# Kernel tuning notes

Measured on AMD Instinct MI355X. Metric: run time of the kernel, lower is better.

## Reference

```python
import jax, jax.numpy as jnp
import numpy as np
from jax import lax

BATCH = 8192
HIDDEN = 128
N_POINTS = 8
MAX_STEPS = 8     # adaptive substep budget per output interval
RTOL, ATOL = 1e-3, 1e-4

# Dormand-Prince 5(4) tableau (FSAL)
A21 = 1/5
A31, A32 = 3/40, 9/40
A41, A42, A43 = 44/45, -56/15, 32/9
A51, A52, A53, A54 = 19372/6561, -25360/2187, 64448/6561, -212/729
A61, A62, A63, A64, A65 = 9017/3168, -355/33, 46732/5247, 49/176, -5103/18656
B1, B3, B4, B5, B6 = 35/384, 500/1113, 125/192, -2187/6784, 11/84
# error weights = b(5th) - b(4th)
E1 = 35/384 - 5179/57600
E3 = 500/1113 - 7571/16695
E4 = 125/192 - 393/640
E5 = -2187/6784 + 92097/339200
E6 = 11/84 - 187/2100
E7 = -1/40


def setup_inputs() -> dict:
    key = jax.random.key(0)
    ks = jax.random.split(key, 6)
    def xavier(k, fi, fo):
        return (jax.random.normal(k, (fi, fo)) * jnp.sqrt(2.0 / (fi + fo))).astype(jnp.float32)
    W1 = xavier(ks[0], 2, HIDDEN); b1 = jnp.zeros((HIDDEN,), jnp.float32)
    W2 = xavier(ks[1], HIDDEN, HIDDEN); b2 = jnp.zeros((HIDDEN,), jnp.float32)
    W3 = xavier(ks[2], HIDDEN, HIDDEN); b3 = jnp.zeros((HIDDEN,), jnp.float32)
    W4 = xavier(ks[3], HIDDEN, 2); b4 = jnp.zeros((2,), jnp.float32)
    x0 = jax.random.normal(ks[4], (BATCH, 2), jnp.float32)
    t = (jnp.arange(N_POINTS, dtype=jnp.float32) * 0.1)
    return {"x0": x0, "t": t, "W1": W1, "b1": b1, "W2": W2, "b2": b2,
            "W3": W3, "b3": b3, "W4": W4, "b4": b4}


def _odeint(x0, t, W1, b1, W2, b2, W3, b3, W4, b4):
    def f(y):  # autonomous dynamics: ODEFunc ignores t
        h = jax.nn.elu(y @ W1 + b1)
        h = jax.nn.elu(h @ W2 + b2)
        h = jax.nn.elu(h @ W3 + b3)
        return h @ W4 + b4

    def dopri5_step(y, h):
        k1 = f(y)
        k2 = f(y + h * (A21 * k1))
        k3 = f(y + h * (A31 * k1 + A32 * k2))
        k4 = f(y + h * (A41 * k1 + A42 * k2 + A43 * k3))
        k5 = f(y + h * (A51 * k1 + A52 * k2 + A53 * k3 + A54 * k4))
        k6 = f(y + h * (A61 * k1 + A62 * k2 + A63 * k3 + A64 * k4 + A65 * k5))
        y5 = y + h * (B1 * k1 + B3 * k3 + B4 * k4 + B5 * k5 + B6 * k6)
        k7 = f(y5)  # FSAL stage, used only for error estimate here
        err = h * (E1 * k1 + E3 * k3 + E4 * k4 + E5 * k5 + E6 * k6 + E7 * k7)
        tol = ATOL + RTOL * jnp.maximum(jnp.abs(y), jnp.abs(y5))
        err_norm = jnp.sqrt(jnp.mean((err / tol) ** 2))
        return y5, err_norm

    def solve_interval(carry, ts):
        y, h = carry
        t0, t1 = ts

        def body(c, _):
            y, tc, h = c
            remaining = t1 - tc
            done = remaining <= 1e-9
            h_eff = jnp.where(done, h, jnp.minimum(h, remaining))
            y5, err_norm = dopri5_step(y, h_eff)
            accept = (err_norm <= 1.0) & (~done)
            y = jnp.where(accept, y5, y)
            tc = jnp.where(accept, tc + h_eff, tc)
            factor = jnp.clip(0.9 * jnp.maximum(err_norm, 1e-10) ** (-0.2), 0.2, 10.0)
            h = jnp.where(done, h, h_eff * factor)
            return (y, tc, h), None

        (y, _, h), _ = lax.scan(body, (y, t0, h), None, length=MAX_STEPS)
        return (y, h), y

    h0 = (t[1] - t[0]) * 0.5
    (_, _), ys = lax.scan(solve_interval, (x0, h0), (t[:-1], t[1:]))
    return jnp.concatenate([x0[None], ys], axis=0)  # (n_points, batch, 2)


def reference(x0, t, W1, b1, W2, b2, W3, b3, W4, b4):
    return _odeint(x0, t, W1, b1, W2, b2, W3, b3, W4, b4)
```

## Files before the change

kernel.cpp:

```cpp
#include <hip/hip_runtime.h>
#include <stdint.h>

typedef unsigned int u32;
typedef unsigned long long u64;
typedef unsigned short u16;
typedef float f32x4 __attribute__((ext_vector_type(4)));
typedef float f32x2 __attribute__((ext_vector_type(2)));
typedef short short8 __attribute__((ext_vector_type(8)));
typedef unsigned int u32x2 __attribute__((ext_vector_type(2)));
typedef unsigned int u32x4 __attribute__((ext_vector_type(4)));

#define HID  128
#define MT   32
#define NWG  256
#define NTHR 512
#define LD   136

#define OFF_ESUM  0
#define OFF_CNT   512
#define OFF_WPACK 8192
#define OFF_W2TH  16384
#define OFF_W3TH  49152

constexpr float CA21 = (float)(1.0/5.0);
constexpr float CA31 = (float)(3.0/40.0),   CA32 = (float)(9.0/40.0);
constexpr float CA41 = (float)(44.0/45.0),  CA42 = (float)(-56.0/15.0), CA43 = (float)(32.0/9.0);
constexpr float CA51 = (float)(19372.0/6561.0), CA52 = (float)(-25360.0/2187.0);
constexpr float CA53 = (float)(64448.0/6561.0), CA54 = (float)(-212.0/729.0);
constexpr float CA61 = (float)(9017.0/3168.0),  CA62 = (float)(-355.0/33.0);
constexpr float CA63 = (float)(46732.0/5247.0), CA64 = (float)(49.0/176.0), CA65 = (float)(-5103.0/18656.0);
constexpr float CB1 = (float)(35.0/384.0), CB3 = (float)(500.0/1113.0), CB4 = (float)(125.0/192.0);
constexpr float CB5 = (float)(-2187.0/6784.0), CB6 = (float)(11.0/84.0);
constexpr float CE1 = (float)(35.0/384.0 - 5179.0/57600.0);
constexpr float CE3 = (float)(500.0/1113.0 - 7571.0/16695.0);
constexpr float CE4 = (float)(125.0/192.0 - 393.0/640.0);
constexpr float CE5 = (float)(-2187.0/6784.0 + 92097.0/339200.0);
constexpr float CE6 = (float)(11.0/84.0 - 187.0/2100.0);
constexpr float CE7 = (float)(-1.0/40.0);

template<int N> struct IC { static constexpr int v = N; };

__device__ __forceinline__ u16 f2bf(float x) {
  u32 u = __builtin_bit_cast(u32, x);
  u32 r = (u + 0x7FFFu + ((u >> 16) & 1u)) >> 16;
  return (u16)r;
}
__device__ __forceinline__ float eluf(float x) {
  return x > 0.f ? x : (__expf(x) - 1.f);
}
__device__ __forceinline__ u32 cvtpk(float a, float b) {
  u32 r; asm("v_cvt_pk_bf16_f32 %0, %1, %2" : "=v"(r) : "v"(a), "v"(b)); return r;
}

__global__ void prologue(const float* __restrict__ x0, const float* __restrict__ t,
                         const float* __restrict__ W1, const float* __restrict__ b1,
                         const float* __restrict__ W2, const float* __restrict__ b2,
                         const float* __restrict__ W3, const float* __restrict__ b3,
                         const float* __restrict__ W4, const float* __restrict__ b4,
                         float* __restrict__ ws, float* __restrict__ out)
{
  int gid = blockIdx.x * blockDim.x + threadIdx.x;
  out[gid] = x0[gid];
  {
    int k = gid >> 7, j = gid & 127;
    u16* w2th = (u16*)((char*)ws + OFF_W2TH);
    u16* w3th = (u16*)((char*)ws + OFF_W3TH);
    w2th[j*HID + k] = f2bf(W2[gid]);
    w3th[j*HID + k] = f2bf(W3[gid]);
  }
  float* wp = ws + OFF_WPACK/4;
  if (gid < 256) wp[gid] = W1[gid];
  if (gid < 128) {
    wp[256 + gid] = b1[gid];
    wp[384 + gid] = b2[gid];
    wp[512 + gid] = b3[gid];
  }
  if (gid < 2)  wp[640 + gid] = b4[gid];
  if (gid < 256) ((u32*)ws)[gid] = 0u;
}

__global__ __launch_bounds__(NTHR, 2)
void solver(const float* __restrict__ x0, const float* __restrict__ t_arr,
            const float* __restrict__ W4g, float* __restrict__ ws,
            float* __restrict__ out)
{
  const int tid  = threadIdx.x;
  const int wg   = blockIdx.x;
  const int lane = tid & 63;
  const int wv   = tid >> 6;
  const int nl   = lane & 15;
  const int g    = lane >> 4;

  __shared__ __align__(16) u16 Ahi[2][MT][LD];
  __shared__ __align__(16) float Wsm[644];
  __shared__ __align__(16) float kS[7][MT][2];
  __shared__ __align__(16) float yL[MT][2];
  __shared__ __align__(16) float y5L[MT][2];
  __shared__ __align__(16) float pD[8][2][16][2];
  __shared__ u32 bcF;
  __shared__ float bcH;

  {
    const float* wp = ws + OFF_WPACK/4;
    Wsm[tid] = wp[tid];
    if (tid < 132) Wsm[512 + tid] = wp[512 + tid];
  }
  if (tid < 64) yL[tid >> 1][tid & 1] = x0[wg*64 + tid];

  const u16* w2th = (const u16*)((const char*)ws + OFF_W2TH);
  const u16* w3th = (const u16*)((const char*)ws + OFF_W3TH);
  short8 W2H[4], W3H[4];
  {
    const int nglob = wv*16 + nl;
#pragma unroll
    for (int ks = 0; ks < 4; ++ks) {
      int off = nglob*HID + ks*32 + g*8;
      W2H[ks] = *(const short8*)(w2th + off);
      W3H[ks] = *(const short8*)(w3th + off);
    }
  }
  float w4c[4][2];
#pragma unroll
  for (int r = 0; r < 4; ++r) {
    int n = wv*16 + g*4 + r;
    w4c[r][0] = W4g[n*2 + 0];
    w4c[r][1] = W4g[n*2 + 1];
  }
  __syncthreads();
  const f32x4 bv2 = *(const f32x4*)&Wsm[384 + wv*16 + g*4];
  const f32x4 bv3 = *(const f32x4*)&Wsm[512 + wv*16 + g*4];

  u64* esum = (u64*)((char*)ws + OFF_ESUM);
  u32* cnt  = (u32*)((char*)ws + OFF_CNT);

  float h = 0.5f * (t_arr[1] - t_arr[0]);
  float heff = h;

  auto phaseA = [&](auto SC, int fromPD) {
    constexpr int S = decltype(SC)::v;
    const int m  = tid >> 4;
    const int jc = tid & 15;
    float ys0, ys1;
    const float y0 = yL[m][0], y1 = yL[m][1];
    if constexpr (S == 1) {
      ys0 = y0; ys1 = y1;
    } else {
      const int mt = m >> 4, ml = m & 15;
      float kp0, kp1;
      if (S == 2 && !fromPD) {
        kp0 = kS[0][m][0]; kp1 = kS[0][m][1];
      } else {
        kp0 = Wsm[640]; kp1 = Wsm[641];
#pragma unroll
        for (int w = 0; w < 8; ++w) {
          f32x2 p = *(const f32x2*)&pD[w][mt][ml][0];
          kp0 += p[0]; kp1 += p[1];
        }
        if (jc < 2) kS[S-2][m][jc] = jc ? kp1 : kp0;
      }
      if constexpr (S == 2) {
        ys0 = fmaf(heff, CA21*kp0, y0);
        ys1 = fmaf(heff, CA21*kp1, y1);
      } else if constexpr (S == 3) {
        f32x2 k1 = *(const f32x2*)&kS[0][m][0];
        ys0 = fmaf(heff, CA31*k1[0] + CA32*kp0, y0);
        ys1 = fmaf(heff, CA31*k1[1] + CA32*kp1, y1);
      } else if constexpr (S == 4) {
        f32x2 k1 = *(const f32x2*)&kS[0][m][0];
        f32x2 k2 = *(const f32x2*)&kS[1][m][0];
        ys0 = fmaf(heff, CA41*k1[0] + CA42*k2[0] + CA43*kp0, y0);
        ys1 = fmaf(heff, CA41*k1[1] + CA42*k2[1] + CA43*kp1, y1);
      } else if constexpr (S == 5) {
        f32x2 k1 = *(const f32x2*)&kS[0][m][0];
        f32x2 k2 = *(const f32x2*)&kS[1][m][0];
        f32x2 k3 = *(const f32x2*)&kS[2][m][0];
        ys0 = fmaf(heff, CA51*k1[0] + CA52*k2[0] + CA53*k3[0] + CA54*kp0, y0);
        ys1 = fmaf(heff, CA51*k1[1] + CA52*k2[1] + CA53*k3[1] + CA54*kp1, y1);
      } else if constexpr (S == 6) {
        f32x2 k1 = *(const f32x2*)&kS[0][m][0];
        f32x2 k2 = *(const f32x2*)&kS[1][m][0];
        f32x2 k3 = *(const f32x2*)&kS[2][m][0];
        f32x2 k4 = *(const f32x2*)&kS[3][m][0];
        ys0 = fmaf(heff, CA61*k1[0] + CA62*k2[0] + CA63*k3[0] + CA64*k4[0] + CA65*kp0, y0);
        ys1 = fmaf(heff, CA61*k1[1] + CA62*k2[1] + CA63*k3[1] + CA64*k4[1] + CA65*kp1, y1);
      } else {
        f32x2 k1 = *(const f32x2*)&kS[0][m][0];
        f32x2 k3 = *(const f32x2*)&kS[2][m][0];
        f32x2 k4 = *(const f32x2*)&kS[3][m][0];
        f32x2 k5 = *(const f32x2*)&kS[4][m][0];
        ys0 = fmaf(heff, CB1*k1[0] + CB3*k3[0] + CB4*k4[0] + CB5*k5[0] + CB6*kp0, y0);
        ys1 = fmaf(heff, CB1*k1[1] + CB3*k3[1] + CB4*k4[1] + CB5*k5[1] + CB6*kp1, y1);
        if (jc < 2) y5L[m][jc] = jc ? ys1 : ys0;
      }
    }
    const int j0 = jc * 8;
    f32x4 w0a = *(const f32x4*)&Wsm[j0],       w0b = *(const f32x4*)&Wsm[j0 + 4];
    f32x4 w1a = *(const f32x4*)&Wsm[128 + j0], w1b = *(const f32x4*)&Wsm[128 + j0 + 4];
    f32x4 ba  = *(const f32x4*)&Wsm[256 + j0], bb  = *(const f32x4*)&Wsm[256 + j0 + 4];
    float v0 = eluf(fmaf(ys1, w1a[0], fmaf(ys0, w0a[0], ba[0])));
    float v1 = eluf(fmaf(ys1, w1a[1], fmaf(ys0, w0a[1], ba[1])));
    float v2 = eluf(fmaf(ys1, w1a[2], fmaf(ys0, w0a[2], ba[2])));
    float v3 = eluf(fmaf(ys1, w1a[3], fmaf(ys0, w0a[3], ba[3])));
    float v4 = eluf(fmaf(ys1, w1b[0], fmaf(ys0, w0b[0], bb[0])));
    float v5 = eluf(fmaf(ys1, w1b[1], fmaf(ys0, w0b[1], bb[1])));
    float v6 = eluf(fmaf(ys1, w1b[2], fmaf(ys0, w0b[2], bb[2])));
    float v7 = eluf(fmaf(ys1, w1b[3], fmaf(ys0, w0b[3], bb[3])));
    u32x4 hp = {cvtpk(v0,v1), cvtpk(v2,v3), cvtpk(v4,v5), cvtpk(v6,v7)};
    *(u32x4*)&Ahi[0][m][j0] = hp;
  };

  auto mmL2 = [&]() {
    f32x4 a0[2];
    a0[0] = bv2; a0[1] = bv2;
#pragma unroll
    for (int ks = 0; ks < 4; ++ks)
#pragma unroll
      for (int mt = 0; mt < 2; ++mt) {
        short8 bh = *(const short8*)&Ahi[0][mt*16 + nl][ks*32 + g*8];
        a0[mt] = __builtin_amdgcn_mfma_f32_16x16x32_bf16(W2H[ks], bh, a0[mt], 0, 0, 0);
      }
    const int n0 = wv*16 + g*4;
#pragma unroll
    for (int mt = 0; mt < 2; ++mt) {
      float v0 = eluf(a0[mt][0]);
      float v1 = eluf(a0[mt][1]);
      float v2 = eluf(a0[mt][2]);
      float v3 = eluf(a0[mt][3]);
      u32x2 hp = {cvtpk(v0, v1), cvtpk(v2, v3)};
      *(u32x2*)&Ahi[1][mt*16 + nl][n0] = hp;
    }
  };

  auto mmL3 = [&]() {
    f32x4 a0[2];
    a0[0] = bv3; a0[1] = bv3;
#pragma unroll
    for (int ks = 0; ks < 4; ++ks)
#pragma unroll
      for (int mt = 0; mt < 2; ++mt) {
        short8 bh = *(const short8*)&Ahi[1][mt*16 + nl][ks*32 + g*8];
        a0[mt] = __builtin_amdgcn_mfma_f32_16x16x32_bf16(W3H[ks], bh, a0[mt], 0, 0, 0);
      }
#pragma unroll
    for (int mt = 0; mt < 2; ++mt) {
      float v0 = eluf(a0[mt][0]);
      float v1 = eluf(a0[mt][1]);
      float v2 = eluf(a0[mt][2]);
      float v3 = eluf(a0[mt][3]);
      float p0 = v0*w4c[0][0] + v1*w4c[1][0] + v2*w4c[2][0] + v3*w4c[3][0];
      float p1 = v0*w4c[0][1] + v1*w4c[1][1] + v2*w4c[2][1] + v3*w4c[3][1];
      p0 += __shfl_xor(p0, 16); p0 += __shfl_xor(p0, 32);
      p1 += __shfl_xor(p1, 16); p1 += __shfl_xor(p1, 32);
      if (lane < 16) {
        f32x2 pp = {p0, p1};
        *(f32x2*)&pD[wv][mt][lane][0] = pp;
      }
    }
  };

  for (int iv = 0; iv < 7; ++iv) {
    const float t1 = t_arr[iv + 1];
    float tc = t_arr[iv];
    for (int s = 0; s < 8; ++s) {
      const int step = iv*8 + s;
      float rem = t1 - tc;
      if (rem <= 1e-9f) break;
      heff = fminf(h, rem);

      if (iv == 0 && s == 0) {
        phaseA(IC<1>{}, 0); __syncthreads();
        mmL2(); __syncthreads();
        mmL3(); __syncthreads();
        phaseA(IC<2>{}, 1);
      } else {
        phaseA(IC<2>{}, 0);
      }
      __syncthreads(); mmL2(); __syncthreads(); mmL3(); __syncthreads();
      phaseA(IC<3>{}, 1); __syncthreads(); mmL2(); __syncthreads(); mmL3(); __syncthreads();
      phaseA(IC<4>{}, 1); __syncthreads(); mmL2(); __syncthreads(); mmL3(); __syncthreads();
      phaseA(IC<5>{}, 1); __syncthreads(); mmL2(); __syncthreads(); mmL3(); __syncthreads();
      phaseA(IC<6>{}, 1); __syncthreads(); mmL2(); __syncthreads(); mmL3(); __syncthreads();
      phaseA(IC<7>{}, 1); __syncthreads(); mmL2(); __syncthreads(); mmL3(); __syncthreads();

      if (wv == 0) {
        int m = lane >> 1, c = lane & 1;
        int emt = m >> 4, eml = m & 15;
        float kp = Wsm[640 + c];
#pragma unroll
        for (int w = 0; w < 8; ++w) kp += pD[w][emt][eml][c];
        kS[6][m][c] = kp;
        float e = heff * (CE1*kS[0][m][c] + CE3*kS[2][m][c] + CE4*kS[3][m][c]
                        + CE5*kS[4][m][c] + CE6*kS[5][m][c] + CE7*kp);
        float tol = 1e-4f + 1e-3f * fmaxf(fabsf(yL[m][c]), fabsf(y5L[m][c]));
        float rr = e / tol;
        float es = rr * rr;
#pragma unroll
        for (int mk = 1; mk < 64; mk <<= 1) es += __shfl_xor(es, mk);
        if (lane == 0) {
          if (!(es < 1e8f)) es = 1e8f;
          u64 q = (u64)(es * 1048576.0f);
          __hip_atomic_fetch_add(&esum[step], q, __ATOMIC_RELAXED, __HIP_MEMORY_SCOPE_AGENT);
          __hip_atomic_fetch_add(&cnt[step], 1u, __ATOMIC_RELEASE, __HIP_MEMORY_SCOPE_AGENT);
        }
      }
      if (tid == 0) {
        while (__hip_atomic_load(&cnt[step], __ATOMIC_ACQUIRE, __HIP_MEMORY_SCOPE_AGENT) < (u32)NWG)
          __builtin_amdgcn_s_sleep(1);
        u64 q = __hip_atomic_load(&esum[step], __ATOMIC_RELAXED, __HIP_MEMORY_SCOPE_AGENT);
        float sum = (float)q * (1.0f/1048576.0f);
        float err_norm = sqrtf(sum * (1.0f/16384.f));
        bool acc = (err_norm <= 1.0f);
        float factor = fminf(10.f, fmaxf(0.2f, 0.9f * powf(fmaxf(err_norm, 1e-10f), -0.2f)));
        bcF = acc ? 1u : 0u;
        bcH = heff * factor;
      }
      __syncthreads();
      {
        bool acc = bcF != 0u;
        if (acc) {
          int m = tid >> 4, jc = tid & 15;
          if (jc < 2) {
            yL[m][jc] = y5L[m][jc];
            kS[0][m][jc] = kS[6][m][jc];
          }
          tc += heff;
        }
        h = bcH;
      }
    }
    __syncthreads();
    if (tid < 64)
      out[(size_t)(iv + 1) * 16384 + wg*64 + tid] = yL[tid >> 1][tid & 1];
  }
}

extern "C" void kernel_launch(void* const* d_in, const int* in_sizes, int n_in,
                              void* d_out, int out_size, void* d_ws, size_t ws_size,
                              hipStream_t stream)
{
  const float* x0 = (const float*)d_in[0];
  const float* t  = (const float*)d_in[1];
  const float* W1 = (const float*)d_in[2];
  const float* b1 = (const float*)d_in[3];
  const float* W2 = (const float*)d_in[4];
  const float* b2 = (const float*)d_in[5];
  const float* W3 = (const float*)d_in[6];
  const float* b3 = (const float*)d_in[7];
  const float* W4 = (const float*)d_in[8];
  const float* b4 = (const float*)d_in[9];
  float* out = (float*)d_out;
  float* ws  = (float*)d_ws;

  prologue<<<64, 256, 0, stream>>>(x0, t, W1, b1, W2, b2, W3, b3, W4, b4, ws, out);
  solver<<<NWG, NTHR, 0, stream>>>(x0, t, W4, ws, out);
}
```

Before: 198.9 us.

## Use two-level tree atomics for grid error reduction and keep RK state in registers

The single per-step global atomic counter that all 256 workgroups hit is replaced by a two-level tree: 16 leaf counters, each padded to its own 64-byte line, pack the error sum and an arrival count into one 64-bit word. The last arriver at each leaf forwards the total to a per-step root word, and every block polls that root. This cuts contention on one address and merges the sum and count into a single atomic. Stage k values and y are also kept in per-thread registers rather than re-read from shared memory, and the final output write drops a barrier. The fixed-point scale of the error sum drops from 2^20 to 2^10, which coarsens its resolution.

```diff
diff --git a/kernel.cpp b/kernel.cpp
--- a/kernel.cpp
+++ b/kernel.cpp
@@ -16,11 +16,11 @@
 #define NTHR 512
 #define LD   136
 
-#define OFF_ESUM  0
-#define OFF_CNT   512
-#define OFF_WPACK 8192
-#define OFF_W2TH  16384
-#define OFF_W3TH  49152
+#define OFF_ROOT  0
+#define OFF_LEAF  4096
+#define OFF_WPACK 61440
+#define OFF_W2TH  65536
+#define OFF_W3TH  98304
 
 constexpr float CA21 = (float)(1.0/5.0);
 constexpr float CA31 = (float)(3.0/40.0),   CA32 = (float)(9.0/40.0);
@@ -76,7 +76,7 @@
     wp[512 + gid] = b3[gid];
   }
   if (gid < 2)  wp[640 + gid] = b4[gid];
-  if (gid < 256) ((u32*)ws)[gid] = 0u;
+  if (gid < 15360) ((u32*)ws)[gid] = 0u;
 }
 
 __global__ __launch_bounds__(NTHR, 2)
@@ -90,13 +90,15 @@
   const int wv   = tid >> 6;
   const int nl   = lane & 15;
   const int g    = lane >> 4;
+  const int m    = tid >> 4;
+  const int jc   = tid & 15;
 
   __shared__ __align__(16) u16 Ahi[2][MT][LD];
   __shared__ __align__(16) float Wsm[644];
-  __shared__ __align__(16) float kS[7][MT][2];
-  __shared__ __align__(16) float yL[MT][2];
-  __shared__ __align__(16) float y5L[MT][2];
-  __shared__ __align__(16) float pD[8][2][16][2];
+  __shared__ __align__(16) float kSm[6][MT][2];
+  __shared__ __align__(16) float yLm[MT][2];
+  __shared__ __align__(16) float y5m[MT][2];
+  __shared__ __align__(16) float pD[8][MT][2];
   __shared__ u32 bcF;
   __shared__ float bcH;
 
@@ -105,7 +107,9 @@
     Wsm[tid] = wp[tid];
     if (tid < 132) Wsm[512 + tid] = wp[512 + tid];
   }
-  if (tid < 64) yL[tid >> 1][tid & 1] = x0[wg*64 + tid];
+  float y0r = x0[wg*64 + m*2 + 0];
+  float y1r = x0[wg*64 + m*2 + 1];
+  if (jc == 0) { yLm[m][0] = y0r; yLm[m][1] = y1r; }
 
   const u16* w2th = (const u16*)((const char*)ws + OFF_W2TH);
   const u16* w3th = (const u16*)((const char*)ws + OFF_W3TH);
@@ -129,68 +133,55 @@
   __syncthreads();
   const f32x4 bv2 = *(const f32x4*)&Wsm[384 + wv*16 + g*4];
   const f32x4 bv3 = *(const f32x4*)&Wsm[512 + wv*16 + g*4];
-
-  u64* esum = (u64*)((char*)ws + OFF_ESUM);
-  u32* cnt  = (u32*)((char*)ws + OFF_CNT);
+  const float b40 = Wsm[640], b41 = Wsm[641];
+
+  float khv[6][2];
+  float y5r0 = 0.f, y5r1 = 0.f;
 
   float h = 0.5f * (t_arr[1] - t_arr[0]);
   float heff = h;
 
-  auto phaseA = [&](auto SC, int fromPD) {
+  auto phaseA = [&](auto SC) {
     constexpr int S = decltype(SC)::v;
-    const int m  = tid >> 4;
-    const int jc = tid & 15;
     float ys0, ys1;
-    const float y0 = yL[m][0], y1 = yL[m][1];
     if constexpr (S == 1) {
-      ys0 = y0; ys1 = y1;
+      ys0 = y0r; ys1 = y1r;
     } else {
-      const int mt = m >> 4, ml = m & 15;
       float kp0, kp1;
-      if (S == 2 && !fromPD) {
-        kp0 = kS[0][m][0]; kp1 = kS[0][m][1];
+      if constexpr (S == 2) {
+        kp0 = khv[0][0]; kp1 = khv[0][1];
       } else {
-        kp0 = Wsm[640]; kp1 = Wsm[641];
+        kp0 = b40; kp1 = b41;
 #pragma unroll
         for (int w = 0; w < 8; ++w) {
-          f32x2 p = *(const f32x2*)&pD[w][mt][ml][0];
+          f32x2 p = *(const f32x2*)&pD[w][m][0];
           kp0 += p[0]; kp1 += p[1];
         }
-        if (jc < 2) kS[S-2][m][jc] = jc ? kp1 : kp0;
+        khv[S-2][0] = kp0; khv[S-2][1] = kp1;
+        if constexpr (S >= 4) {
+          if (jc == 0) { kSm[S-2][m][0] = kp0; kSm[S-2][m][1] = kp1; }
+        }
       }
       if constexpr (S == 2) {
-        ys0 = fmaf(heff, CA21*kp0, y0);
-        ys1 = fmaf(heff, CA21*kp1, y1);
+        ys0 = fmaf(heff, CA21*kp0, y0r);
+        ys1 = fmaf(heff, CA21*kp1, y1r);
       } else if constexpr (S == 3) {
-        f32x2 k1 = *(const f32x2*)&kS[0][m][0];
-        ys0 = fmaf(heff, CA31*k1[0] + CA32*kp0, y0);
-        ys1 = fmaf(heff, CA31*k1[1] + CA32*kp1, y1);
+        ys0 = fmaf(heff, CA31*khv[0][0] + CA32*kp0, y0r);
+        ys1 = fmaf(heff, CA31*khv[0][1] + CA32*kp1, y1r);
       } else if constexpr (S == 4) {
-        f32x2 k1 = *(const f32x2*)&kS[0][m][0];
-        f32x2 k2 = *(const f32x2*)&kS[1][m][0];
-        ys0 = fmaf(heff, CA41*k1[0] + CA42*k2[0] + CA43*kp0, y0);
-        ys1 = fmaf(heff, CA41*k1[1] + CA42*k2[1] + CA43*kp1, y1);
+        ys0 = fmaf(heff, CA41*khv[0][0] + CA42*khv[1][0] + CA43*kp0, y0r);
+        ys1 = fmaf(heff, CA41*khv[0][1] + CA42*khv[1][1] + CA43*kp1, y1r);
       } else if constexpr (S == 5) {
-        f32x2 k1 = *(const f32x2*)&kS[0][m][0];
-        f32x2 k2 = *(const f32x2*)&kS[1][m][0];
-        f32x2 k3 = *(const f32x2*)&kS[2][m][0];
-        ys0 = fmaf(heff, CA51*k1[0] + CA52*k2[0] + CA53*k3[0] + CA54*kp0, y0);
-        ys1 = fmaf(heff, CA51*k1[1] + CA52*k2[1] + CA53*k3[1] + CA54*kp1, y1);
+        ys0 = fmaf(heff, CA51*khv[0][0] + CA52*khv[1][0] + CA53*khv[2][0] + CA54*kp0, y0r);
+        ys1 = fmaf(heff, CA51*khv[0][1] + CA52*khv[1][1] + CA53*khv[2][1] + CA54*kp1, y1r);
       } else if constexpr (S == 6) {
-        f32x2 k1 = *(const f32x2*)&kS[0][m][0];
-        f32x2 k2 = *(const f32x2*)&kS[1][m][0];
-        f32x2 k3 = *(const f32x2*)&kS[2][m][0];
-        f32x2 k4 = *(const f32x2*)&kS[3][m][0];
-        ys0 = fmaf(heff, CA61*k1[0] + CA62*k2[0] + CA63*k3[0] + CA64*k4[0] + CA65*kp0, y0);
-        ys1 = fmaf(heff, CA61*k1[1] + CA62*k2[1] + CA63*k3[1] + CA64*k4[1] + CA65*kp1, y1);
+        ys0 = fmaf(heff, CA61*khv[0][0] + CA62*khv[1][0] + CA63*khv[2][0] + CA64*khv[3][0] + CA65*kp0, y0r);
+        ys1 = fmaf(heff, CA61*khv[0][1] + CA62*khv[1][1] + CA63*khv[2][1] + CA64*khv[3][1] + CA65*kp1, y1r);
       } else {
-        f32x2 k1 = *(const f32x2*)&kS[0][m][0];
-        f32x2 k3 = *(const f32x2*)&kS[2][m][0];
-        f32x2 k4 = *(const f32x2*)&kS[3][m][0];
-        f32x2 k5 = *(const f32x2*)&kS[4][m][0];
-        ys0 = fmaf(heff, CB1*k1[0] + CB3*k3[0] + CB4*k4[0] + CB5*k5[0] + CB6*kp0, y0);
-        ys1 = fmaf(heff, CB1*k1[1] + CB3*k3[1] + CB4*k4[1] + CB5*k5[1] + CB6*kp1, y1);
-        if (jc < 2) y5L[m][jc] = jc ? ys1 : ys0;
+        ys0 = fmaf(heff, CB1*khv[0][0] + CB3*khv[2][0] + CB4*khv[3][0] + CB5*khv[4][0] + CB6*kp0, y0r);
+        ys1 = fmaf(heff, CB1*khv[0][1] + CB3*khv[2][1] + CB4*khv[3][1] + CB5*khv[4][1] + CB6*kp1, y1r);
+        y5r0 = ys0; y5r1 = ys1;
+        if (jc == 0) { y5m[m][0] = ys0; y5m[m][1] = ys1; }
       }
     }
     const int j0 = jc * 8;
@@ -253,7 +244,7 @@
       p1 += __shfl_xor(p1, 16); p1 += __shfl_xor(p1, 32);
       if (lane < 16) {
         f32x2 pp = {p0, p1};
-        *(f32x2*)&pD[wv][mt][lane][0] = pp;
+        *(f32x2*)&pD[wv][mt*16 + lane][0] = pp;
       }
     }
   };
@@ -268,46 +259,63 @@
       heff = fminf(h, rem);
 
       if (iv == 0 && s == 0) {
-        phaseA(IC<1>{}, 0); __syncthreads();
+        phaseA(IC<1>{}); __syncthreads();
         mmL2(); __syncthreads();
         mmL3(); __syncthreads();
-        phaseA(IC<2>{}, 1);
-      } else {
-        phaseA(IC<2>{}, 0);
-      }
-      __syncthreads(); mmL2(); __syncthreads(); mmL3(); __syncthreads();
-      phaseA(IC<3>{}, 1); __syncthreads(); mmL2(); __syncthreads(); mmL3(); __syncthreads();
-      phaseA(IC<4>{}, 1); __syncthreads(); mmL2(); __syncthreads(); mmL3(); __syncthreads();
-      phaseA(IC<5>{}, 1); __syncthreads(); mmL2(); __syncthreads(); mmL3(); __syncthreads();
-      phaseA(IC<6>{}, 1); __syncthreads(); mmL2(); __syncthreads(); mmL3(); __syncthreads();
-      phaseA(IC<7>{}, 1); __syncthreads(); mmL2(); __syncthreads(); mmL3(); __syncthreads();
+        float kp0 = b40, kp1 = b41;
+#pragma unroll
+        for (int w = 0; w < 8; ++w) {
+          f32x2 p = *(const f32x2*)&pD[w][m][0];
+          kp0 += p[0]; kp1 += p[1];
+        }
+        khv[0][0] = kp0; khv[0][1] = kp1;
+        if (jc == 0) { kSm[0][m][0] = kp0; kSm[0][m][1] = kp1; }
+      }
+      phaseA(IC<2>{}); __syncthreads(); mmL2(); __syncthreads(); mmL3(); __syncthreads();
+      phaseA(IC<3>{}); __syncthreads(); mmL2(); __syncthreads(); mmL3(); __syncthreads();
+      phaseA(IC<4>{}); __syncthreads(); mmL2(); __syncthreads(); mmL3(); __syncthreads();
+      phaseA(IC<5>{}); __syncthreads(); mmL2(); __syncthreads(); mmL3(); __syncthreads();
+      phaseA(IC<6>{}); __syncthreads(); mmL2(); __syncthreads(); mmL3(); __syncthreads();
+      phaseA(IC<7>{}); __syncthreads(); mmL2(); __syncthreads(); mmL3(); __syncthreads();
 
       if (wv == 0) {
-        int m = lane >> 1, c = lane & 1;
-        int emt = m >> 4, eml = m & 15;
-        float kp = Wsm[640 + c];
-#pragma unroll
-        for (int w = 0; w < 8; ++w) kp += pD[w][emt][eml][c];
-        kS[6][m][c] = kp;
-        float e = heff * (CE1*kS[0][m][c] + CE3*kS[2][m][c] + CE4*kS[3][m][c]
-                        + CE5*kS[4][m][c] + CE6*kS[5][m][c] + CE7*kp);
-        float tol = 1e-4f + 1e-3f * fmaxf(fabsf(yL[m][c]), fabsf(y5L[m][c]));
+        int em = lane >> 1, ec = lane & 1;
+        float kp = ec ? b41 : b40;
+#pragma unroll
+        for (int w = 0; w < 8; ++w) kp += pD[w][em][ec];
+        float e = heff * (CE1*kSm[0][em][ec] + CE3*kSm[2][em][ec] + CE4*kSm[3][em][ec]
+                        + CE5*kSm[4][em][ec] + CE6*kSm[5][em][ec] + CE7*kp);
+        float tol = 1e-4f + 1e-3f * fmaxf(fabsf(yLm[em][ec]), fabsf(y5m[em][ec]));
         float rr = e / tol;
         float es = rr * rr;
 #pragma unroll
         for (int mk = 1; mk < 64; mk <<= 1) es += __shfl_xor(es, mk);
         if (lane == 0) {
-          if (!(es < 1e8f)) es = 1e8f;
-          u64 q = (u64)(es * 1048576.0f);
-          __hip_atomic_fetch_add(&esum[step], q, __ATOMIC_RELAXED, __HIP_MEMORY_SCOPE_AGENT);
-          __hip_atomic_fetch_add(&cnt[step], 1u, __ATOMIC_RELEASE, __HIP_MEMORY_SCOPE_AGENT);
-        }
+          if (!(es < 1e9f)) es = 1e9f;
+          u64 q = (u64)(es * 1024.0f);
+          u64 add = (q << 10) | 1ULL;
+          u64* leaf = (u64*)((char*)ws + OFF_LEAF + ((size_t)step*16 + (wg & 15))*64);
+          u64 old = __hip_atomic_fetch_add(leaf, add, __ATOMIC_ACQ_REL, __HIP_MEMORY_SCOPE_AGENT);
+          if ((old & 0x3FFULL) == 15ULL) {
+            u64 tot = old + add;
+            u64 radd = ((tot >> 10) << 10) | 1ULL;
+            u64* rootp = (u64*)((char*)ws + OFF_ROOT + (size_t)step*64);
+            __hip_atomic_fetch_add(rootp, radd, __ATOMIC_ACQ_REL, __HIP_MEMORY_SCOPE_AGENT);
+          }
+        }
+      }
+      float k7p0 = b40, k7p1 = b41;
+#pragma unroll
+      for (int w = 0; w < 8; ++w) {
+        f32x2 p = *(const f32x2*)&pD[w][m][0];
+        k7p0 += p[0]; k7p1 += p[1];
       }
       if (tid == 0) {
-        while (__hip_atomic_load(&cnt[step], __ATOMIC_ACQUIRE, __HIP_MEMORY_SCOPE_AGENT) < (u32)NWG)
+        u64* rootp = (u64*)((char*)ws + OFF_ROOT + (size_t)step*64);
+        u64 v;
+        while (((v = __hip_atomic_load(rootp, __ATOMIC_ACQUIRE, __HIP_MEMORY_SCOPE_AGENT)) & 0x3FFULL) != 16ULL)
           __builtin_amdgcn_s_sleep(1);
-        u64 q = __hip_atomic_load(&esum[step], __ATOMIC_RELAXED, __HIP_MEMORY_SCOPE_AGENT);
-        float sum = (float)q * (1.0f/1048576.0f);
+        float sum = (float)(v >> 10) * (1.0f/1024.0f);
         float err_norm = sqrtf(sum * (1.0f/16384.f));
         bool acc = (err_norm <= 1.0f);
         float factor = fminf(10.f, fmaxf(0.2f, 0.9f * powf(fmaxf(err_norm, 1e-10f), -0.2f)));
@@ -318,19 +326,21 @@
       {
         bool acc = bcF != 0u;
         if (acc) {
-          int m = tid >> 4, jc = tid & 15;
-          if (jc < 2) {
-            yL[m][jc] = y5L[m][jc];
-            kS[0][m][jc] = kS[6][m][jc];
+          y0r = y5r0; y1r = y5r1;
+          khv[0][0] = k7p0; khv[0][1] = k7p1;
+          if (jc == 0) {
+            kSm[0][m][0] = k7p0; kSm[0][m][1] = k7p1;
+            yLm[m][0] = y5r0;    yLm[m][1] = y5r1;
           }
           tc += heff;
         }
         h = bcH;
       }
     }
-    __syncthreads();
-    if (tid < 64)
-      out[(size_t)(iv + 1) * 16384 + wg*64 + tid] = yL[tid >> 1][tid & 1];
+    if (jc == 0) {
+      f32x2 yo = {y0r, y1r};
+      *(f32x2*)&out[(size_t)(iv + 1) * 16384 + wg*64 + m*2] = yo;
+    }
   }
 }
 
```

New measurement: 173.3 us. 12.9% less time.
